# Kernel optimization log

Measured on AMD Instinct MI355X. Metric: run time of the kernel, lower is better.

Reference implementation:

```python
import jax, jax.numpy as jnp
import numpy as np

B, L, H2, P, A, T = 2048, 128, 600, 50, 50, 3  # batch, seq, 2*hidden, pos_emb, attn, latent types


def setup_inputs() -> dict:
    key = jax.random.key(0)
    ks = jax.random.split(key, 9)
    return {
        "hidden": jax.random.normal(ks[0], (B, L, H2), dtype=jnp.float32),
        "pos1_emb": jax.random.normal(ks[1], (B, L, P), dtype=jnp.float32),
        "pos2_emb": jax.random.normal(ks[2], (B, L, P), dtype=jnp.float32),
        "entity1_idx": jax.random.randint(ks[3], (B,), 0, L),
        "entity2_idx": jax.random.randint(ks[4], (B,), 0, L),
        "W_hid": jax.random.normal(ks[5], (A, H2 + 2 * P), dtype=jnp.float32) * 0.05,
        "W_ent": jax.random.normal(ks[6], (A, 4 * H2), dtype=jnp.float32) * 0.05,
        "latent_types": jax.random.normal(ks[7], (T, H2), dtype=jnp.float32) * 0.05,
        "v": jax.random.normal(ks[8], (A, 1), dtype=jnp.float32) * 0.05,
    }


def _latent_type(ent, latent_types):
    # ent: [B, 1, H2]; latent_types: [T, H2]
    a = jax.nn.softmax(jnp.einsum("bed,td->bet", ent, latent_types), axis=-1)
    return jnp.einsum("bet,td->bed", a, latent_types)  # [B, 1, H2]


def reference(hidden, pos1_emb, pos2_emb, entity1_idx, entity2_idx, W_hid, W_ent, latent_types, v):
    b = hidden.shape[0]
    batch_ix = jnp.arange(b)
    hid_e1 = hidden[batch_ix, entity1_idx][:, None, :]  # [B, 1, H2]
    hid_e2 = hidden[batch_ix, entity2_idx][:, None, :]
    e1_type = _latent_type(hid_e1, latent_types)
    e2_type = _latent_type(hid_e2, latent_types)
    # u1: per-token projection, u2: per-sentence entity projection (broadcast over L)
    u1 = jnp.einsum("bld,ad->bla", jnp.concatenate([hidden, pos1_emb, pos2_emb], axis=-1), W_hid)
    u2 = jnp.einsum("bed,ad->bea", jnp.concatenate([hid_e1, e1_type, hid_e2, e2_type], axis=-1), W_ent)
    u = jnp.tanh(u1 + u2)  # [B, L, A]
    scores = jnp.einsum("bla,a->bl", u, v[:, 0])  # [B, L]
    alpha = jax.nn.softmax(scores, axis=-1)
    z = jnp.einsum("bl,bld->bd", alpha, hidden)  # [B, H2]
    return z
```

## Files before the change

### kernel.cpp

```cpp
#include <hip/hip_runtime.h>
#include <hip/hip_bf16.h>
#include <math.h>


#define B_    2048
#define L_    128
#define H2_   600
#define P_    50
#define A_    50
#define D700  700
#define KCN   22
#define KHALF 11
#define AP    64
#define MT    16
#define XP    712

typedef __attribute__((ext_vector_type(8))) short short8;
typedef __attribute__((ext_vector_type(4))) float f32x4;

__device__ __forceinline__ unsigned short f2bf(float f) {
  unsigned u = __float_as_uint(f);
  u += 0x7fffu + ((u >> 16) & 1u);
  return (unsigned short)(u >> 16);
}
__device__ __forceinline__ unsigned cvtpk(float a, float b) {
  unsigned r;
  asm("v_cvt_pk_bf16_f32 %0, %1, %2" : "=v"(r) : "v"(a), "v"(b));
  return r;
}
__device__ __forceinline__ float bf2f(unsigned short s) {
  return __uint_as_float(((unsigned)s) << 16);
}

__global__ __launch_bounds__(256) void kwprep(const float* __restrict__ Wh,
                                              unsigned short* __restrict__ Wt) {
  int idx = blockIdx.x * 256 + threadIdx.x;
  if (idx >= KCN * 2048) return;
  int kc = idx >> 11, r = idx & 2047, a = r >> 5, kk = r & 31;
  int d = kc * 32 + kk;
  float v = (a < A_ && d < D700) ? Wh[a * D700 + d] : 0.f;
  Wt[idx] = f2bf(v);
}

__global__ __launch_bounds__(256) void ku2(const float* __restrict__ hidden,
                                           const int* __restrict__ e1,
                                           const int* __restrict__ e2,
                                           const float* __restrict__ Went,
                                           const float* __restrict__ lt,
                                           float* __restrict__ u2ws) {
  __shared__ __align__(16) float E[2][2400];
  __shared__ float dots[2][2][3];
  __shared__ float aw[2][2][3];
  int tid = threadIdx.x;
  int b0 = blockIdx.x * 2;

  for (int idx = tid; idx < 2 * 2 * 150; idx += 256) {
    int i = idx / 300, r = idx - i * 300, e = r / 150, g = r - e * 150;
    int bb = b0 + i;
    int l = e ? e2[bb] : e1[bb];
    float4 f = *(const float4*)(hidden + ((size_t)bb * L_ + l) * H2_ + g * 4);
    *(float4*)(&E[i][e * 1200 + g * 4]) = f;
  }
  __syncthreads();

  int w = tid >> 6, lane = tid & 63;
  for (int task = w * 3; task < w * 3 + 3; ++task) {
    int i = task / 6, e = (task / 3) & 1, t = task % 3;
    float p = 0.f;
    for (int d = lane; d < 600; d += 64) p += E[i][e * 1200 + d] * lt[t * 600 + d];
    #pragma unroll
    for (int mask = 1; mask <= 32; mask <<= 1) p += __shfl_xor(p, mask);
    if (lane == 0) dots[i][e][t] = p;
  }
  __syncthreads();
  if (tid < 12) {
    int t = tid % 3, e = (tid / 3) & 1, i = tid / 6;
    float d0 = dots[i][e][0], d1 = dots[i][e][1], d2 = dots[i][e][2];
    float m = fmaxf(d0, fmaxf(d1, d2));
    float x0 = expf(d0 - m), x1 = expf(d1 - m), x2 = expf(d2 - m);
    float Z = x0 + x1 + x2;
    aw[i][e][t] = ((t == 0) ? x0 : (t == 1) ? x1 : x2) / Z;
  }
  __syncthreads();
  for (int idx = tid; idx < 2 * 2 * 600; idx += 256) {
    int i = idx / 1200, r = idx - i * 1200, e = r / 600, d = r - e * 600;
    float v = aw[i][e][0] * lt[d] + aw[i][e][1] * lt[600 + d] + aw[i][e][2] * lt[1200 + d];
    E[i][e * 1200 + 600 + d] = v;
  }
  __syncthreads();
  for (int a = w; a < A_; a += 4) {
    float acc[2] = {0.f, 0.f};
    for (int d0 = lane * 4; d0 < 2400; d0 += 256) {
      float4 wv = *(const float4*)(Went + a * 2400 + d0);
      #pragma unroll
      for (int i = 0; i < 2; ++i) {
        float4 ev = *(const float4*)(&E[i][d0]);
        acc[i] += ev.x * wv.x + ev.y * wv.y + ev.z * wv.z + ev.w * wv.w;
      }
    }
    #pragma unroll
    for (int i = 0; i < 2; ++i) {
      float p = acc[i];
      #pragma unroll
      for (int mask = 1; mask <= 32; mask <<= 1) p += __shfl_xor(p, mask);
      if (lane == 0) u2ws[(b0 + i) * AP + a] = p;
    }
  }
  for (int idx = tid; idx < 2 * (AP - A_); idx += 256) {
    u2ws[(b0 + idx / (AP - A_)) * AP + A_ + idx % (AP - A_)] = 0.f;
  }
}

__global__ __launch_bounds__(512, 6) void kmain(
    const float* __restrict__ hidden, const float* __restrict__ pos1,
    const float* __restrict__ pos2, const float* __restrict__ vvec,
    const unsigned short* __restrict__ Wt, const float* __restrict__ u2ws,
    float* __restrict__ zp_ws, float* __restrict__ mS_ws) {
  __shared__ __align__(16) unsigned short Xs[MT * XP];
  __shared__ __align__(16) float pacc[4][64][4];
  __shared__ float scores4[4][MT];
  __shared__ float es_s[MT];
  __shared__ float u2s[AP];
  __shared__ float vs[AP];

  int tid = threadIdx.x;
  int bq = blockIdx.x;
  int b = bq >> 3, tok0 = (bq & 7) * MT;
  int w = tid >> 6, lane = tid & 63;
  int acol = lane & 15, kgrp = lane >> 4;

  int t = tid >> 5, c0 = tid & 31;
  const float* rowp = hidden + ((size_t)(b * L_ + tok0) + t) * H2_;
  float4 f[4];
  #pragma unroll
  for (int j = 0; j < 4; ++j) f[j] = *(const float4*)(rowp + (c0 + 32 * j) * 4);
  bool h5 = (c0 < 22);
  float4 f4;
  if (h5) f4 = *(const float4*)(rowp + (c0 + 128) * 4);

  const float* p1 = pos1 + (size_t)(b * L_ + tok0) * P_;
  const float* p2 = pos2 + (size_t)(b * L_ + tok0) * P_;
  bool hp = (tid < 400);
  float2 q1, q2;
  if (hp) {
    q1 = *(const float2*)(p1 + tid * 2);
    q2 = *(const float2*)(p2 + tid * 2);
  }
  float u2v = 0.f, vvv = 0.f;
  if (tid < AP) {
    u2v = u2ws[b * AP + tid];
    vvv = (tid < A_) ? vvec[tid] : 0.f;
  }

  #pragma unroll
  for (int j = 0; j < 4; ++j) {
    uint2 wv2; wv2.x = cvtpk(f[j].x, f[j].y); wv2.y = cvtpk(f[j].z, f[j].w);
    *(uint2*)(&Xs[t * XP + (c0 + 32 * j) * 4]) = wv2;
  }
  if (h5) {
    uint2 wv2; wv2.x = cvtpk(f4.x, f4.y); wv2.y = cvtpk(f4.z, f4.w);
    *(uint2*)(&Xs[t * XP + (c0 + 128) * 4]) = wv2;
  }
  if (hp) {
    int t1 = tid / 25, g = tid - t1 * 25;
    *(unsigned*)(&Xs[t1 * XP + 600 + g * 2]) = cvtpk(q1.x, q1.y);
    *(unsigned*)(&Xs[t1 * XP + 650 + g * 2]) = cvtpk(q2.x, q2.y);
  }
  if (tid < MT) {
    uint2 zz; zz.x = 0u; zz.y = 0u;
    *(uint2*)(&Xs[tid * XP + 700]) = zz;
  }
  if (tid < AP) { u2s[tid] = u2v; vs[tid] = vvv; }
  __syncthreads();

  int at = w & 3;
  int kc0 = (w >> 2) * KHALF;
  const unsigned short* wbase = Wt + (at * 16 + acol) * 32 + kgrp * 8;
  short8 wf[KHALF];
  #pragma unroll
  for (int kc = 0; kc < KHALF; ++kc)
    wf[kc] = *(const short8*)(wbase + (kc0 + kc) * 2048);

  f32x4 acc = {0.f, 0.f, 0.f, 0.f};
  #pragma unroll
  for (int kc = 0; kc < KHALF; ++kc) {
    short8 a0 = *(const short8*)(&Xs[acol * XP + (kc0 + kc) * 32 + kgrp * 8]);
    acc = __builtin_amdgcn_mfma_f32_16x16x32_bf16(a0, wf[kc], acc, 0, 0, 0);
  }

  if (w >= 4) {
    float4 pv = {acc[0], acc[1], acc[2], acc[3]};
    *(float4*)(&pacc[w - 4][lane][0]) = pv;
  }
  __syncthreads();
  if (w < 4) {
    float va = vs[w * 16 + acol];
    float u2a = u2s[w * 16 + acol];
    float4 pv = *(const float4*)(&pacc[w][lane][0]);
    float s0[4];
    s0[0] = va * tanhf(acc[0] + pv.x + u2a);
    s0[1] = va * tanhf(acc[1] + pv.y + u2a);
    s0[2] = va * tanhf(acc[2] + pv.z + u2a);
    s0[3] = va * tanhf(acc[3] + pv.w + u2a);
    #pragma unroll
    for (int mask = 1; mask < 16; mask <<= 1) {
      #pragma unroll
      for (int r = 0; r < 4; ++r) s0[r] += __shfl_xor(s0[r], mask);
    }
    if (acol == 0) {
      #pragma unroll
      for (int r = 0; r < 4; ++r) scores4[w][kgrp * 4 + r] = s0[r];
    }
  }
  __syncthreads();

  if (tid < 64) {
    float s = (tid < MT)
                  ? (scores4[0][tid] + scores4[1][tid] + scores4[2][tid] + scores4[3][tid])
                  : -3.402823466e38f;
    float m = s;
    #pragma unroll
    for (int mask = 1; mask <= 32; mask <<= 1) m = fmaxf(m, __shfl_xor(m, mask));
    float e = (tid < MT) ? expf(s - m) : 0.f;
    float S = e;
    #pragma unroll
    for (int mask = 1; mask <= 32; mask <<= 1) S += __shfl_xor(S, mask);
    if (tid < MT) es_s[tid] = e;
    if (tid == 0) { mS_ws[bq * 2] = m; mS_ws[bq * 2 + 1] = S; }
  }
  __syncthreads();

  if (tid < 150) {
    float z0 = 0.f, z1 = 0.f, z2 = 0.f, z3 = 0.f;
    #pragma unroll
    for (int r = 0; r < MT; ++r) {
      uint2 xv = *(const uint2*)(&Xs[r * XP + tid * 4]);
      float e = es_s[r];
      z0 += e * bf2f((unsigned short)(xv.x & 0xffff));
      z1 += e * bf2f((unsigned short)(xv.x >> 16));
      z2 += e * bf2f((unsigned short)(xv.y & 0xffff));
      z3 += e * bf2f((unsigned short)(xv.y >> 16));
    }
    float4 wv = {z0, z1, z2, z3};
    *(float4*)(zp_ws + (size_t)bq * 600 + tid * 4) = wv;
  }
}

__global__ __launch_bounds__(128) void kcomb(const float* __restrict__ zp_ws,
                                             const float* __restrict__ mS_ws,
                                             float* __restrict__ out) {
  int b = blockIdx.x, tid = threadIdx.x;
  float mq[8], Sq[8];
  #pragma unroll
  for (int qq = 0; qq < 8; ++qq) {
    mq[qq] = mS_ws[(b * 8 + qq) * 2];
    Sq[qq] = mS_ws[(b * 8 + qq) * 2 + 1];
  }
  float M = mq[0];
  #pragma unroll
  for (int qq = 1; qq < 8; ++qq) M = fmaxf(M, mq[qq]);
  float c[8], Z = 0.f;
  #pragma unroll
  for (int qq = 0; qq < 8; ++qq) { c[qq] = expf(mq[qq] - M); Z += Sq[qq] * c[qq]; }
  float inv = 1.f / Z;
  for (int d = tid; d < 600; d += 128) {
    float z = 0.f;
    #pragma unroll
    for (int qq = 0; qq < 8; ++qq) z += c[qq] * zp_ws[(size_t)(b * 8 + qq) * 600 + d];
    out[b * 600 + d] = z * inv;
  }
}

extern "C" void kernel_launch(void* const* d_in, const int* in_sizes, int n_in,
                              void* d_out, int out_size, void* d_ws, size_t ws_size,
                              hipStream_t stream) {
  const float* hidden = (const float*)d_in[0];
  const float* pos1   = (const float*)d_in[1];
  const float* pos2   = (const float*)d_in[2];
  const int*   e1     = (const int*)d_in[3];
  const int*   e2     = (const int*)d_in[4];
  const float* Whid   = (const float*)d_in[5];
  const float* Went   = (const float*)d_in[6];
  const float* lt     = (const float*)d_in[7];
  const float* vvec   = (const float*)d_in[8];
  float* out = (float*)d_out;

  char* ws = (char*)d_ws;
  unsigned short* Wt = (unsigned short*)ws;
  float* u2ws  = (float*)(ws + 98304);
  float* mS_ws = (float*)(ws + 98304 + 524288);
  float* zp_ws = (float*)(ws + 98304 + 524288 + 131072);

  hipLaunchKernelGGL(kwprep, dim3(176), dim3(256), 0, stream, Whid, Wt);
  hipLaunchKernelGGL(ku2, dim3(B_ / 2), dim3(256), 0, stream, hidden, e1, e2, Went, lt, u2ws);
  hipLaunchKernelGGL(kmain, dim3(B_ * 8), dim3(512), 0, stream, hidden, pos1, pos2, vvec,
                     Wt, u2ws, zp_ws, mS_ws);
  hipLaunchKernelGGL(kcomb, dim3(B_), dim3(128), 0, stream, zp_ws, mS_ws, out);
}
```

Baseline: 263.9 us.

## Process two token tiles per block with prefetch of second tile during first

Each kmain block now handles two consecutive 16-token tiles using double-buffered LDS. The second tile's global loads are issued while the first tile's MFMA and softmax run, and the W fragments are loaded once and reused for both tiles. The aim is to hide global load latency and halve the weight-fragment loads per tile. In exchange it uses more LDS and registers, lowers the occupancy hint from 6 to 4 and halves the grid size.

```diff
diff --git a/kernel.cpp b/kernel.cpp
--- a/kernel.cpp
+++ b/kernel.cpp
@@ -111,68 +111,48 @@
   }
 }
 
-__global__ __launch_bounds__(512, 6) void kmain(
+__global__ __launch_bounds__(512, 4) void kmain(
     const float* __restrict__ hidden, const float* __restrict__ pos1,
     const float* __restrict__ pos2, const float* __restrict__ vvec,
     const unsigned short* __restrict__ Wt, const float* __restrict__ u2ws,
     float* __restrict__ zp_ws, float* __restrict__ mS_ws) {
-  __shared__ __align__(16) unsigned short Xs[MT * XP];
+  __shared__ __align__(16) unsigned short Xs[2][MT * XP];
   __shared__ __align__(16) float pacc[4][64][4];
   __shared__ float scores4[4][MT];
   __shared__ float es_s[MT];
-  __shared__ float u2s[AP];
+  __shared__ float u2s[2][AP];
   __shared__ float vs[AP];
 
   int tid = threadIdx.x;
-  int bq = blockIdx.x;
-  int b = bq >> 3, tok0 = (bq & 7) * MT;
+  int T0 = blockIdx.x * 2, T1 = T0 + 1;
+  int b0 = T0 >> 3, tok00 = (T0 & 7) * MT;
+  int b1 = T1 >> 3, tok01 = (T1 & 7) * MT;
   int w = tid >> 6, lane = tid & 63;
   int acol = lane & 15, kgrp = lane >> 4;
 
   int t = tid >> 5, c0 = tid & 31;
-  const float* rowp = hidden + ((size_t)(b * L_ + tok0) + t) * H2_;
-  float4 f[4];
-  #pragma unroll
-  for (int j = 0; j < 4; ++j) f[j] = *(const float4*)(rowp + (c0 + 32 * j) * 4);
   bool h5 = (c0 < 22);
-  float4 f4;
-  if (h5) f4 = *(const float4*)(rowp + (c0 + 128) * 4);
-
-  const float* p1 = pos1 + (size_t)(b * L_ + tok0) * P_;
-  const float* p2 = pos2 + (size_t)(b * L_ + tok0) * P_;
   bool hp = (tid < 400);
-  float2 q1, q2;
+
+  const float* rowp0 = hidden + ((size_t)(b0 * L_ + tok00) + t) * H2_;
+  float4 f0[4];
+  #pragma unroll
+  for (int j = 0; j < 4; ++j) f0[j] = *(const float4*)(rowp0 + (c0 + 32 * j) * 4);
+  float4 f04;
+  if (h5) f04 = *(const float4*)(rowp0 + (c0 + 128) * 4);
+  const float* p10 = pos1 + (size_t)(b0 * L_ + tok00) * P_;
+  const float* p20 = pos2 + (size_t)(b0 * L_ + tok00) * P_;
+  float2 q10, q20;
   if (hp) {
-    q1 = *(const float2*)(p1 + tid * 2);
-    q2 = *(const float2*)(p2 + tid * 2);
-  }
-  float u2v = 0.f, vvv = 0.f;
+    q10 = *(const float2*)(p10 + tid * 2);
+    q20 = *(const float2*)(p20 + tid * 2);
+  }
+  float u2v0 = 0.f, u2v1 = 0.f, vvv = 0.f;
   if (tid < AP) {
-    u2v = u2ws[b * AP + tid];
+    u2v0 = u2ws[b0 * AP + tid];
+    u2v1 = u2ws[b1 * AP + tid];
     vvv = (tid < A_) ? vvec[tid] : 0.f;
   }
-
-  #pragma unroll
-  for (int j = 0; j < 4; ++j) {
-    uint2 wv2; wv2.x = cvtpk(f[j].x, f[j].y); wv2.y = cvtpk(f[j].z, f[j].w);
-    *(uint2*)(&Xs[t * XP + (c0 + 32 * j) * 4]) = wv2;
-  }
-  if (h5) {
-    uint2 wv2; wv2.x = cvtpk(f4.x, f4.y); wv2.y = cvtpk(f4.z, f4.w);
-    *(uint2*)(&Xs[t * XP + (c0 + 128) * 4]) = wv2;
-  }
-  if (hp) {
-    int t1 = tid / 25, g = tid - t1 * 25;
-    *(unsigned*)(&Xs[t1 * XP + 600 + g * 2]) = cvtpk(q1.x, q1.y);
-    *(unsigned*)(&Xs[t1 * XP + 650 + g * 2]) = cvtpk(q2.x, q2.y);
-  }
-  if (tid < MT) {
-    uint2 zz; zz.x = 0u; zz.y = 0u;
-    *(uint2*)(&Xs[tid * XP + 700]) = zz;
-  }
-  if (tid < AP) { u2s[tid] = u2v; vs[tid] = vvv; }
-  __syncthreads();
-
   int at = w & 3;
   int kc0 = (w >> 2) * KHALF;
   const unsigned short* wbase = Wt + (at * 16 + acol) * 32 + kgrp * 8;
@@ -181,10 +161,46 @@
   for (int kc = 0; kc < KHALF; ++kc)
     wf[kc] = *(const short8*)(wbase + (kc0 + kc) * 2048);
 
+  #pragma unroll
+  for (int j = 0; j < 4; ++j) {
+    uint2 wv2; wv2.x = cvtpk(f0[j].x, f0[j].y); wv2.y = cvtpk(f0[j].z, f0[j].w);
+    *(uint2*)(&Xs[0][t * XP + (c0 + 32 * j) * 4]) = wv2;
+  }
+  if (h5) {
+    uint2 wv2; wv2.x = cvtpk(f04.x, f04.y); wv2.y = cvtpk(f04.z, f04.w);
+    *(uint2*)(&Xs[0][t * XP + (c0 + 128) * 4]) = wv2;
+  }
+  if (hp) {
+    int t1 = tid / 25, g = tid - t1 * 25;
+    *(unsigned*)(&Xs[0][t1 * XP + 600 + g * 2]) = cvtpk(q10.x, q10.y);
+    *(unsigned*)(&Xs[0][t1 * XP + 650 + g * 2]) = cvtpk(q20.x, q20.y);
+  }
+  if (tid < MT * 2) {
+    int hh = tid >> 4;
+    uint2 zz; zz.x = 0u; zz.y = 0u;
+    *(uint2*)(&Xs[hh][(tid & 15) * XP + 700]) = zz;
+  }
+  if (tid < AP) { u2s[0][tid] = u2v0; u2s[1][tid] = u2v1; vs[tid] = vvv; }
+  __syncthreads();
+
+  const float* rowp1 = hidden + ((size_t)(b1 * L_ + tok01) + t) * H2_;
+  float4 g1[4];
+  #pragma unroll
+  for (int j = 0; j < 4; ++j) g1[j] = *(const float4*)(rowp1 + (c0 + 32 * j) * 4);
+  float4 g14;
+  if (h5) g14 = *(const float4*)(rowp1 + (c0 + 128) * 4);
+  const float* p11 = pos1 + (size_t)(b1 * L_ + tok01) * P_;
+  const float* p21 = pos2 + (size_t)(b1 * L_ + tok01) * P_;
+  float2 q11, q21;
+  if (hp) {
+    q11 = *(const float2*)(p11 + tid * 2);
+    q21 = *(const float2*)(p21 + tid * 2);
+  }
+
   f32x4 acc = {0.f, 0.f, 0.f, 0.f};
   #pragma unroll
   for (int kc = 0; kc < KHALF; ++kc) {
-    short8 a0 = *(const short8*)(&Xs[acol * XP + (kc0 + kc) * 32 + kgrp * 8]);
+    short8 a0 = *(const short8*)(&Xs[0][acol * XP + (kc0 + kc) * 32 + kgrp * 8]);
     acc = __builtin_amdgcn_mfma_f32_16x16x32_bf16(a0, wf[kc], acc, 0, 0, 0);
   }
 
@@ -195,7 +211,7 @@
   __syncthreads();
   if (w < 4) {
     float va = vs[w * 16 + acol];
-    float u2a = u2s[w * 16 + acol];
+    float u2a = u2s[0][w * 16 + acol];
     float4 pv = *(const float4*)(&pacc[w][lane][0]);
     float s0[4];
     s0[0] = va * tanhf(acc[0] + pv.x + u2a);
@@ -213,7 +229,6 @@
     }
   }
   __syncthreads();
-
   if (tid < 64) {
     float s = (tid < MT)
                   ? (scores4[0][tid] + scores4[1][tid] + scores4[2][tid] + scores4[3][tid])
@@ -226,15 +241,29 @@
     #pragma unroll
     for (int mask = 1; mask <= 32; mask <<= 1) S += __shfl_xor(S, mask);
     if (tid < MT) es_s[tid] = e;
-    if (tid == 0) { mS_ws[bq * 2] = m; mS_ws[bq * 2 + 1] = S; }
-  }
-  __syncthreads();
-
+    if (tid == 0) { mS_ws[T0 * 2] = m; mS_ws[T0 * 2 + 1] = S; }
+  }
+  __syncthreads();
+
+  #pragma unroll
+  for (int j = 0; j < 4; ++j) {
+    uint2 wv2; wv2.x = cvtpk(g1[j].x, g1[j].y); wv2.y = cvtpk(g1[j].z, g1[j].w);
+    *(uint2*)(&Xs[1][t * XP + (c0 + 32 * j) * 4]) = wv2;
+  }
+  if (h5) {
+    uint2 wv2; wv2.x = cvtpk(g14.x, g14.y); wv2.y = cvtpk(g14.z, g14.w);
+    *(uint2*)(&Xs[1][t * XP + (c0 + 128) * 4]) = wv2;
+  }
+  if (hp) {
+    int t1 = tid / 25, g = tid - t1 * 25;
+    *(unsigned*)(&Xs[1][t1 * XP + 600 + g * 2]) = cvtpk(q11.x, q11.y);
+    *(unsigned*)(&Xs[1][t1 * XP + 650 + g * 2]) = cvtpk(q21.x, q21.y);
+  }
   if (tid < 150) {
     float z0 = 0.f, z1 = 0.f, z2 = 0.f, z3 = 0.f;
     #pragma unroll
     for (int r = 0; r < MT; ++r) {
-      uint2 xv = *(const uint2*)(&Xs[r * XP + tid * 4]);
+      uint2 xv = *(const uint2*)(&Xs[0][r * XP + tid * 4]);
       float e = es_s[r];
       z0 += e * bf2f((unsigned short)(xv.x & 0xffff));
       z1 += e * bf2f((unsigned short)(xv.x >> 16));
@@ -242,7 +271,69 @@
       z3 += e * bf2f((unsigned short)(xv.y >> 16));
     }
     float4 wv = {z0, z1, z2, z3};
-    *(float4*)(zp_ws + (size_t)bq * 600 + tid * 4) = wv;
+    *(float4*)(zp_ws + (size_t)T0 * 600 + tid * 4) = wv;
+  }
+  __syncthreads();
+
+  f32x4 acc1 = {0.f, 0.f, 0.f, 0.f};
+  #pragma unroll
+  for (int kc = 0; kc < KHALF; ++kc) {
+    short8 a0 = *(const short8*)(&Xs[1][acol * XP + (kc0 + kc) * 32 + kgrp * 8]);
+    acc1 = __builtin_amdgcn_mfma_f32_16x16x32_bf16(a0, wf[kc], acc1, 0, 0, 0);
+  }
+  if (w >= 4) {
+    float4 pv = {acc1[0], acc1[1], acc1[2], acc1[3]};
+    *(float4*)(&pacc[w - 4][lane][0]) = pv;
+  }
+  __syncthreads();
+  if (w < 4) {
+    float va = vs[w * 16 + acol];
+    float u2a = u2s[1][w * 16 + acol];
+    float4 pv = *(const float4*)(&pacc[w][lane][0]);
+    float s0[4];
+    s0[0] = va * tanhf(acc1[0] + pv.x + u2a);
+    s0[1] = va * tanhf(acc1[1] + pv.y + u2a);
+    s0[2] = va * tanhf(acc1[2] + pv.z + u2a);
+    s0[3] = va * tanhf(acc1[3] + pv.w + u2a);
+    #pragma unroll
+    for (int mask = 1; mask < 16; mask <<= 1) {
+      #pragma unroll
+      for (int r = 0; r < 4; ++r) s0[r] += __shfl_xor(s0[r], mask);
+    }
+    if (acol == 0) {
+      #pragma unroll
+      for (int r = 0; r < 4; ++r) scores4[w][kgrp * 4 + r] = s0[r];
+    }
+  }
+  __syncthreads();
+  if (tid < 64) {
+    float s = (tid < MT)
+                  ? (scores4[0][tid] + scores4[1][tid] + scores4[2][tid] + scores4[3][tid])
+                  : -3.402823466e38f;
+    float m = s;
+    #pragma unroll
+    for (int mask = 1; mask <= 32; mask <<= 1) m = fmaxf(m, __shfl_xor(m, mask));
+    float e = (tid < MT) ? expf(s - m) : 0.f;
+    float S = e;
+    #pragma unroll
+    for (int mask = 1; mask <= 32; mask <<= 1) S += __shfl_xor(S, mask);
+    if (tid < MT) es_s[tid] = e;
+    if (tid == 0) { mS_ws[T1 * 2] = m; mS_ws[T1 * 2 + 1] = S; }
+  }
+  __syncthreads();
+  if (tid < 150) {
+    float z0 = 0.f, z1 = 0.f, z2 = 0.f, z3 = 0.f;
+    #pragma unroll
+    for (int r = 0; r < MT; ++r) {
+      uint2 xv = *(const uint2*)(&Xs[1][r * XP + tid * 4]);
+      float e = es_s[r];
+      z0 += e * bf2f((unsigned short)(xv.x & 0xffff));
+      z1 += e * bf2f((unsigned short)(xv.x >> 16));
+      z2 += e * bf2f((unsigned short)(xv.y & 0xffff));
+      z3 += e * bf2f((unsigned short)(xv.y >> 16));
+    }
+    float4 wv = {z0, z1, z2, z3};
+    *(float4*)(zp_ws + (size_t)T1 * 600 + tid * 4) = wv;
   }
 }
 
@@ -293,7 +384,7 @@
 
   hipLaunchKernelGGL(kwprep, dim3(176), dim3(256), 0, stream, Whid, Wt);
   hipLaunchKernelGGL(ku2, dim3(B_ / 2), dim3(256), 0, stream, hidden, e1, e2, Went, lt, u2ws);
-  hipLaunchKernelGGL(kmain, dim3(B_ * 8), dim3(512), 0, stream, hidden, pos1, pos2, vvec,
+  hipLaunchKernelGGL(kmain, dim3(B_ * 4), dim3(512), 0, stream, hidden, pos1, pos2, vvec,
                      Wt, u2ws, zp_ws, mS_ws);
   hipLaunchKernelGGL(kcomb, dim3(B_), dim3(128), 0, stream, zp_ws, mS_ws, out);
 }
```

New measurement: 256.2 us. -2.9%, faster.

## Double token tile to 32 per block, reusing W fragments across two MFMAs

Applied to the files above, without the earlier changes.

Each kmain block now processes 32 tokens instead of 16, halving the grid and issuing two MFMAs per loaded W fragment so the register-held weights are reused across both token halves. The per-block partial softmax count drops from 8 to 4, shrinking the zp/mS workspace traffic and the combine kernel's work. The W fragment loads are moved before the barrier to overlap with staging. Shared memory per block grows, and the launch bound changes from 6 to 4 blocks per CU, lowering occupancy.

```diff
diff --git a/kernel.cpp b/kernel.cpp
--- a/kernel.cpp
+++ b/kernel.cpp
@@ -12,7 +12,7 @@
 #define KCN   22
 #define KHALF 11
 #define AP    64
-#define MT    16
+#define MT    32
 #define XP    712
 
 typedef __attribute__((ext_vector_type(8))) short short8;
@@ -111,40 +111,42 @@
   }
 }
 
-__global__ __launch_bounds__(512, 6) void kmain(
+__global__ __launch_bounds__(512, 4) void kmain(
     const float* __restrict__ hidden, const float* __restrict__ pos1,
     const float* __restrict__ pos2, const float* __restrict__ vvec,
     const unsigned short* __restrict__ Wt, const float* __restrict__ u2ws,
     float* __restrict__ zp_ws, float* __restrict__ mS_ws) {
   __shared__ __align__(16) unsigned short Xs[MT * XP];
-  __shared__ __align__(16) float pacc[4][64][4];
+  __shared__ __align__(16) float pacc[4][64][8];
   __shared__ float scores4[4][MT];
   __shared__ float es_s[MT];
   __shared__ float u2s[AP];
   __shared__ float vs[AP];
 
   int tid = threadIdx.x;
-  int bq = blockIdx.x;
-  int b = bq >> 3, tok0 = (bq & 7) * MT;
+  int T = blockIdx.x;
+  int b = T >> 2, tok0 = (T & 3) * MT;
   int w = tid >> 6, lane = tid & 63;
   int acol = lane & 15, kgrp = lane >> 4;
 
-  int t = tid >> 5, c0 = tid & 31;
+  int t = tid >> 4, c0 = tid & 15;
   const float* rowp = hidden + ((size_t)(b * L_ + tok0) + t) * H2_;
-  float4 f[4];
-  #pragma unroll
-  for (int j = 0; j < 4; ++j) f[j] = *(const float4*)(rowp + (c0 + 32 * j) * 4);
-  bool h5 = (c0 < 22);
-  float4 f4;
-  if (h5) f4 = *(const float4*)(rowp + (c0 + 128) * 4);
+  float4 f[9];
+  #pragma unroll
+  for (int j = 0; j < 9; ++j) f[j] = *(const float4*)(rowp + (c0 + 16 * j) * 4);
+  bool h10 = (c0 < 6);
+  float4 f9;
+  if (h10) f9 = *(const float4*)(rowp + (c0 + 144) * 4);
 
   const float* p1 = pos1 + (size_t)(b * L_ + tok0) * P_;
   const float* p2 = pos2 + (size_t)(b * L_ + tok0) * P_;
-  bool hp = (tid < 400);
-  float2 q1, q2;
-  if (hp) {
-    q1 = *(const float2*)(p1 + tid * 2);
-    q2 = *(const float2*)(p2 + tid * 2);
+  float2 q1a = *(const float2*)(p1 + tid * 2);
+  float2 q2a = *(const float2*)(p2 + tid * 2);
+  bool hq = (tid < 288);
+  float2 q1b, q2b;
+  if (hq) {
+    q1b = *(const float2*)(p1 + (tid + 512) * 2);
+    q2b = *(const float2*)(p2 + (tid + 512) * 2);
   }
   float u2v = 0.f, vvv = 0.f;
   if (tid < AP) {
@@ -153,25 +155,30 @@
   }
 
   #pragma unroll
-  for (int j = 0; j < 4; ++j) {
+  for (int j = 0; j < 9; ++j) {
     uint2 wv2; wv2.x = cvtpk(f[j].x, f[j].y); wv2.y = cvtpk(f[j].z, f[j].w);
-    *(uint2*)(&Xs[t * XP + (c0 + 32 * j) * 4]) = wv2;
-  }
-  if (h5) {
-    uint2 wv2; wv2.x = cvtpk(f4.x, f4.y); wv2.y = cvtpk(f4.z, f4.w);
-    *(uint2*)(&Xs[t * XP + (c0 + 128) * 4]) = wv2;
-  }
-  if (hp) {
+    *(uint2*)(&Xs[t * XP + (c0 + 16 * j) * 4]) = wv2;
+  }
+  if (h10) {
+    uint2 wv2; wv2.x = cvtpk(f9.x, f9.y); wv2.y = cvtpk(f9.z, f9.w);
+    *(uint2*)(&Xs[t * XP + (c0 + 144) * 4]) = wv2;
+  }
+  {
     int t1 = tid / 25, g = tid - t1 * 25;
-    *(unsigned*)(&Xs[t1 * XP + 600 + g * 2]) = cvtpk(q1.x, q1.y);
-    *(unsigned*)(&Xs[t1 * XP + 650 + g * 2]) = cvtpk(q2.x, q2.y);
+    *(unsigned*)(&Xs[t1 * XP + 600 + g * 2]) = cvtpk(q1a.x, q1a.y);
+    *(unsigned*)(&Xs[t1 * XP + 650 + g * 2]) = cvtpk(q2a.x, q2a.y);
+  }
+  if (hq) {
+    int idx = tid + 512;
+    int t1 = idx / 25, g = idx - t1 * 25;
+    *(unsigned*)(&Xs[t1 * XP + 600 + g * 2]) = cvtpk(q1b.x, q1b.y);
+    *(unsigned*)(&Xs[t1 * XP + 650 + g * 2]) = cvtpk(q2b.x, q2b.y);
   }
   if (tid < MT) {
     uint2 zz; zz.x = 0u; zz.y = 0u;
     *(uint2*)(&Xs[tid * XP + 700]) = zz;
   }
   if (tid < AP) { u2s[tid] = u2v; vs[tid] = vvv; }
-  __syncthreads();
 
   int at = w & 3;
   int kc0 = (w >> 2) * KHALF;
@@ -180,36 +187,53 @@
   #pragma unroll
   for (int kc = 0; kc < KHALF; ++kc)
     wf[kc] = *(const short8*)(wbase + (kc0 + kc) * 2048);
-
-  f32x4 acc = {0.f, 0.f, 0.f, 0.f};
+  __syncthreads();
+
+  f32x4 acc0 = {0.f, 0.f, 0.f, 0.f}, acc1 = {0.f, 0.f, 0.f, 0.f};
   #pragma unroll
   for (int kc = 0; kc < KHALF; ++kc) {
-    short8 a0 = *(const short8*)(&Xs[acol * XP + (kc0 + kc) * 32 + kgrp * 8]);
-    acc = __builtin_amdgcn_mfma_f32_16x16x32_bf16(a0, wf[kc], acc, 0, 0, 0);
+    int ke = (kc0 + kc) * 32 + kgrp * 8;
+    short8 a0 = *(const short8*)(&Xs[acol * XP + ke]);
+    short8 a1 = *(const short8*)(&Xs[(16 + acol) * XP + ke]);
+    acc0 = __builtin_amdgcn_mfma_f32_16x16x32_bf16(a0, wf[kc], acc0, 0, 0, 0);
+    acc1 = __builtin_amdgcn_mfma_f32_16x16x32_bf16(a1, wf[kc], acc1, 0, 0, 0);
   }
 
   if (w >= 4) {
-    float4 pv = {acc[0], acc[1], acc[2], acc[3]};
-    *(float4*)(&pacc[w - 4][lane][0]) = pv;
+    float4 pv0 = {acc0[0], acc0[1], acc0[2], acc0[3]};
+    float4 pv1 = {acc1[0], acc1[1], acc1[2], acc1[3]};
+    *(float4*)(&pacc[w - 4][lane][0]) = pv0;
+    *(float4*)(&pacc[w - 4][lane][4]) = pv1;
   }
   __syncthreads();
   if (w < 4) {
     float va = vs[w * 16 + acol];
     float u2a = u2s[w * 16 + acol];
-    float4 pv = *(const float4*)(&pacc[w][lane][0]);
-    float s0[4];
-    s0[0] = va * tanhf(acc[0] + pv.x + u2a);
-    s0[1] = va * tanhf(acc[1] + pv.y + u2a);
-    s0[2] = va * tanhf(acc[2] + pv.z + u2a);
-    s0[3] = va * tanhf(acc[3] + pv.w + u2a);
+    float4 pv0 = *(const float4*)(&pacc[w][lane][0]);
+    float4 pv1 = *(const float4*)(&pacc[w][lane][4]);
+    float s0[4], s1[4];
+    s0[0] = va * tanhf(acc0[0] + pv0.x + u2a);
+    s0[1] = va * tanhf(acc0[1] + pv0.y + u2a);
+    s0[2] = va * tanhf(acc0[2] + pv0.z + u2a);
+    s0[3] = va * tanhf(acc0[3] + pv0.w + u2a);
+    s1[0] = va * tanhf(acc1[0] + pv1.x + u2a);
+    s1[1] = va * tanhf(acc1[1] + pv1.y + u2a);
+    s1[2] = va * tanhf(acc1[2] + pv1.z + u2a);
+    s1[3] = va * tanhf(acc1[3] + pv1.w + u2a);
     #pragma unroll
     for (int mask = 1; mask < 16; mask <<= 1) {
       #pragma unroll
-      for (int r = 0; r < 4; ++r) s0[r] += __shfl_xor(s0[r], mask);
+      for (int r = 0; r < 4; ++r) {
+        s0[r] += __shfl_xor(s0[r], mask);
+        s1[r] += __shfl_xor(s1[r], mask);
+      }
     }
     if (acol == 0) {
       #pragma unroll
-      for (int r = 0; r < 4; ++r) scores4[w][kgrp * 4 + r] = s0[r];
+      for (int r = 0; r < 4; ++r) {
+        scores4[w][kgrp * 4 + r] = s0[r];
+        scores4[w][16 + kgrp * 4 + r] = s1[r];
+      }
     }
   }
   __syncthreads();
@@ -226,7 +250,7 @@
     #pragma unroll
     for (int mask = 1; mask <= 32; mask <<= 1) S += __shfl_xor(S, mask);
     if (tid < MT) es_s[tid] = e;
-    if (tid == 0) { mS_ws[bq * 2] = m; mS_ws[bq * 2 + 1] = S; }
+    if (tid == 0) { mS_ws[T * 2] = m; mS_ws[T * 2 + 1] = S; }
   }
   __syncthreads();
 
@@ -242,7 +266,7 @@
       z3 += e * bf2f((unsigned short)(xv.y >> 16));
     }
     float4 wv = {z0, z1, z2, z3};
-    *(float4*)(zp_ws + (size_t)bq * 600 + tid * 4) = wv;
+    *(float4*)(zp_ws + (size_t)T * 600 + tid * 4) = wv;
   }
 }
 
@@ -250,23 +274,21 @@
                                              const float* __restrict__ mS_ws,
                                              float* __restrict__ out) {
   int b = blockIdx.x, tid = threadIdx.x;
-  float mq[8], Sq[8];
-  #pragma unroll
-  for (int qq = 0; qq < 8; ++qq) {
-    mq[qq] = mS_ws[(b * 8 + qq) * 2];
-    Sq[qq] = mS_ws[(b * 8 + qq) * 2 + 1];
-  }
-  float M = mq[0];
-  #pragma unroll
-  for (int qq = 1; qq < 8; ++qq) M = fmaxf(M, mq[qq]);
-  float c[8], Z = 0.f;
-  #pragma unroll
-  for (int qq = 0; qq < 8; ++qq) { c[qq] = expf(mq[qq] - M); Z += Sq[qq] * c[qq]; }
+  float mq[4], Sq[4];
+  #pragma unroll
+  for (int qq = 0; qq < 4; ++qq) {
+    mq[qq] = mS_ws[(b * 4 + qq) * 2];
+    Sq[qq] = mS_ws[(b * 4 + qq) * 2 + 1];
+  }
+  float M = fmaxf(fmaxf(mq[0], mq[1]), fmaxf(mq[2], mq[3]));
+  float c[4], Z = 0.f;
+  #pragma unroll
+  for (int qq = 0; qq < 4; ++qq) { c[qq] = expf(mq[qq] - M); Z += Sq[qq] * c[qq]; }
   float inv = 1.f / Z;
   for (int d = tid; d < 600; d += 128) {
     float z = 0.f;
     #pragma unroll
-    for (int qq = 0; qq < 8; ++qq) z += c[qq] * zp_ws[(size_t)(b * 8 + qq) * 600 + d];
+    for (int qq = 0; qq < 4; ++qq) z += c[qq] * zp_ws[(size_t)(b * 4 + qq) * 600 + d];
     out[b * 600 + d] = z * inv;
   }
 }
@@ -293,7 +315,7 @@
 
   hipLaunchKernelGGL(kwprep, dim3(176), dim3(256), 0, stream, Whid, Wt);
   hipLaunchKernelGGL(ku2, dim3(B_ / 2), dim3(256), 0, stream, hidden, e1, e2, Went, lt, u2ws);
-  hipLaunchKernelGGL(kmain, dim3(B_ * 8), dim3(512), 0, stream, hidden, pos1, pos2, vvec,
+  hipLaunchKernelGGL(kmain, dim3(B_ * 4), dim3(512), 0, stream, hidden, pos1, pos2, vvec,
                      Wt, u2ws, zp_ws, mS_ws);
   hipLaunchKernelGGL(kcomb, dim3(B_), dim3(128), 0, stream, zp_ws, mS_ws, out);
 }
```

New measurement: 244.0 us. 1.08x faster.
